# Optimization experiments

Measured on AMD Instinct MI355X. Metric: run time of the kernel, lower is better.

## Reference

```python
import jax, jax.numpy as jnp
import numpy as np

G = 32            # gridsize
N = G * G         # num_nodes = 1024
F_IN = 32         # input_dim
H = 256           # hidden_dim
L = 4             # n_layers
B = 64            # batch
MID = F_IN + L * H
MIN_VAL = -10000000.0
EPS_LN = 1e-5
EPS_BN = 1e-5


def _grid_edges():
    ids = np.arange(N).reshape(G, G)
    hs, hd = ids[:, :-1].ravel(), ids[:, 1:].ravel()
    vs, vd = ids[:-1, :].ravel(), ids[1:, :].ravel()
    src = np.concatenate([hs, hd, vs, vd]).astype(np.int32)
    dst = np.concatenate([hd, hs, vd, vs]).astype(np.int32)
    return jnp.asarray(src), jnp.asarray(dst)


def setup_inputs() -> dict:
    key = jax.random.key(0)
    ks = jax.random.split(key, 16)
    mask_f = jax.random.bernoulli(ks[0], 0.7, (B, N)).astype(jnp.float32)
    feats = jax.random.normal(ks[1], (B, N * F_IN), dtype=jnp.float32)
    observations = jnp.concatenate([mask_f, feats], axis=1)
    src, dst = _grid_edges()
    def lin(k, fi, fo):
        return jax.random.normal(k, (fi, fo), dtype=jnp.float32) / np.sqrt(fi)
    W0 = lin(ks[2], F_IN, H); b0 = jnp.zeros((H,), jnp.float32)
    g0 = jnp.ones((H,), jnp.float32); be0 = jnp.zeros((H,), jnp.float32)
    Ws = jax.random.normal(ks[3], (L - 1, H, H), jnp.float32) / np.sqrt(H)
    bs = jnp.zeros((L - 1, H), jnp.float32)
    gs = jnp.ones((L - 1, H), jnp.float32); bes = jnp.zeros((L - 1, H), jnp.float32)
    W1 = lin(ks[4], MID, 2 * H); b1 = jnp.zeros((2 * H,), jnp.float32)
    bn_g = jnp.ones((2 * H,), jnp.float32); bn_b = jnp.zeros((2 * H,), jnp.float32)
    bn_m = jax.random.normal(ks[5], (2 * H,), jnp.float32) * 0.1
    bn_v = jax.random.uniform(ks[6], (2 * H,), jnp.float32, 0.5, 1.5)
    W2 = lin(ks[7], 2 * H, 1); b2 = jnp.zeros((1,), jnp.float32)
    return {"observations": observations, "src": src, "dst": dst,
            "W0": W0, "b0": b0, "g0": g0, "be0": be0,
            "Ws": Ws, "bs": bs, "gs": gs, "bes": bes,
            "W1": W1, "b1": b1, "bn_g": bn_g, "bn_b": bn_b,
            "bn_m": bn_m, "bn_v": bn_v, "W2": W2, "b2": b2}


def _layer_norm(z, g, b):
    mu = z.mean(-1, keepdims=True)
    var = z.var(-1, keepdims=True)
    return (z - mu) / jnp.sqrt(var + EPS_LN) * g + b


def reference(observations, src, dst, W0, b0, g0, be0, Ws, bs, gs, bes,
              W1, b1, bn_g, bn_b, bn_m, bn_v, W2, b2):
    mask = observations[:, :N] != 0.0                      # [B,N] bool action mask
    x = observations[:, N:].reshape(B, N, F_IN)            # node features
    outs = [x]
    h = x
    for l in range(L):
        # GIN with eps=-1: (1+eps)*x_i vanishes -> mlp(sum of neighbor features)
        agg = jnp.zeros_like(h).at[:, dst, :].add(h[:, src, :])
        W, bb, g, be = ((W0, b0, g0, be0) if l == 0
                        else (Ws[l - 1], bs[l - 1], gs[l - 1], bes[l - 1]))
        h = jax.nn.relu(_layer_norm(agg @ W + bb, g, be))  # mlp ReLU; outer .relu() is idempotent
        outs.append(h)
    xc = jnp.concatenate(outs, axis=-1).reshape(B * N, MID)
    z = xc @ W1 + b1
    z = (z - bn_m) / jnp.sqrt(bn_v + EPS_BN) * bn_g + bn_b  # BatchNorm1d eval mode
    z = jax.nn.relu(z)                                       # dropout off in eval
    y = (z @ W2 + b2).reshape(B, N)
    return jnp.where(mask, y, MIN_VAL)
```

## Files before the change

### kernel.cpp

```cpp
#include <hip/hip_runtime.h>
#include <stdint.h>

#define FIN 32
#define HD 256
#define MIDK 1056
#define HF 512
#define MROWS 65536
#define OBS_STRIDE 33792

typedef float f32x2 __attribute__((ext_vector_type(2)));
typedef float f32x4 __attribute__((ext_vector_type(4)));

__device__ __forceinline__ unsigned pack4fp8(float a, float b, float c, float d) {
    int w = __builtin_amdgcn_cvt_pk_fp8_f32(a, b, 0, false);
    return (unsigned)__builtin_amdgcn_cvt_pk_fp8_f32(c, d, w, true);
}
__device__ __forceinline__ unsigned char f2fp8(float f) {
    return (unsigned char)(__builtin_amdgcn_cvt_pk_fp8_f32(f, f, 0, false) & 0xff);
}

__device__ __forceinline__ void glds16(const void* g, void* l) {
    __builtin_amdgcn_global_load_lds(
        (const __attribute__((address_space(1))) unsigned int*)g,
        (__attribute__((address_space(3))) unsigned int*)l,
        16, 0, 0);
}

__device__ __forceinline__ void gather16(const float* __restrict__ src, int stride, int n,
                                         unsigned char* __restrict__ dst) {
    float f[16];
#pragma unroll
    for (int j = 0; j < 16; ++j) f[j] = src[(size_t)j * stride + n];
    uint4 o;
    o.x = pack4fp8(f[0],  f[1],  f[2],  f[3]);
    o.y = pack4fp8(f[4],  f[5],  f[6],  f[7]);
    o.z = pack4fp8(f[8],  f[9],  f[10], f[11]);
    o.w = pack4fp8(f[12], f[13], f[14], f[15]);
    *(uint4*)dst = o;
}

__global__ __launch_bounds__(256) void k_prep_w(
        const float* __restrict__ W0, const float* __restrict__ Ws,
        const float* __restrict__ W1,
        unsigned char* __restrict__ Wt0, unsigned char* __restrict__ WtL,
        unsigned char* __restrict__ WtF) {
    const int b = blockIdx.x, t = threadIdx.x;
    if (b < 2) {
        int s = b * 256 + t;
        int hh = s >> 8, n = s & 255;
        gather16(W0 + (size_t)(hh * 16) * HD, HD, n, Wt0 + (size_t)s * 16);
    } else if (b < 50) {
        int u = (b - 2) * 256 + t;
        int l = u >> 12, s = u & 4095;
        int kb = s >> 9, hh = (s >> 8) & 1, n = s & 255;
        gather16(Ws + (size_t)l * 65536 + (size_t)(kb * 32 + hh * 16) * HD, HD, n,
                 WtL + (size_t)l * 65536 + (size_t)s * 16);
    } else {
        int s = (b - 50) * 256 + t;
        int kb = s >> 11, hh = (s >> 9) & 3, n = s & 511;
        int k0 = kb * 64 + hh * 16;
        if (k0 < MIDK)
            gather16(W1 + (size_t)k0 * HF, HF, n, WtF + (size_t)s * 16);
        else
            *(uint4*)(WtF + (size_t)s * 16) = make_uint4(0, 0, 0, 0);
    }
}

template <int K>
__global__ __launch_bounds__(256, 4) void k_layer(
        const unsigned char* __restrict__ Hin,
        const float* __restrict__ obs,
        const unsigned char* __restrict__ Wt,
        const float* __restrict__ bias, const float* __restrict__ gamma,
        const float* __restrict__ beta, unsigned char* __restrict__ Hout) {
    constexpr int KB = K / 32;
    __shared__ __align__(16) unsigned char Agg[(K / 16) * 64 * 16];
    __shared__ float ls[64], lss[64];
    const int t = threadIdx.x;
    const int w = t >> 6, lane = t & 63, quad = lane >> 4, l15 = lane & 15;
    const int q1 = quad >> 1, q0 = quad & 1;
    const int m0 = ((blockIdx.x & 7) * 128 + (blockIdx.x >> 3)) * 64;
    if (t < 64) { ls[t] = 0.f; lss[t] = 0.f; }

    if constexpr (K == 256) {
        const int r32 = t >> 3, seg = t & 7;
        const size_t rowBase = (size_t)(m0 & ~1023);
#pragma unroll
        for (int p = 0; p < 2; ++p) {
            const int r = p * 32 + r32;
            const int node = (m0 + r) & 1023;
            const int rr = node >> 5, cc = node & 31;
            float s[32];
#pragma unroll
            for (int i = 0; i < 32; ++i) s[i] = 0.f;
            auto addn = [&](int nn) {
                const uint4* pp = (const uint4*)(Hin + (rowBase + nn) * (size_t)K + seg * 32);
                uint4 u0 = pp[0], u1 = pp[1];
                unsigned uu[8] = {u0.x, u0.y, u0.z, u0.w, u1.x, u1.y, u1.z, u1.w};
#pragma unroll
                for (int i = 0; i < 8; ++i) {
                    f32x2 lo = __builtin_amdgcn_cvt_pk_f32_fp8(uu[i], false);
                    f32x2 hi = __builtin_amdgcn_cvt_pk_f32_fp8(uu[i], true);
                    s[4 * i + 0] += lo.x; s[4 * i + 1] += lo.y;
                    s[4 * i + 2] += hi.x; s[4 * i + 3] += hi.y;
                }
            };
            if (cc > 0)  addn(node - 1);
            if (cc < 31) addn(node + 1);
            if (rr > 0)  addn(node - 32);
            if (rr < 31) addn(node + 32);
            unsigned ow[8];
#pragma unroll
            for (int i = 0; i < 8; ++i)
                ow[i] = pack4fp8(s[4 * i], s[4 * i + 1], s[4 * i + 2], s[4 * i + 3]);
            ((uint4*)Agg)[(2 * seg) * 64 + r]     = make_uint4(ow[0], ow[1], ow[2], ow[3]);
            ((uint4*)Agg)[(2 * seg + 1) * 64 + r] = make_uint4(ow[4], ow[5], ow[6], ow[7]);
        }
    } else {
        const int r = t >> 2, seg4 = t & 3;
        const int bimg = m0 >> 10;
        const int node = (m0 + r) & 1023;
        const int rr = node >> 5, cc = node & 31;
        const float* fb = obs + (size_t)bimg * OBS_STRIDE + 1024 + seg4 * 8;
        float s[8] = {0, 0, 0, 0, 0, 0, 0, 0};
        auto addnf = [&](int nn) {
            const float4* fp = (const float4*)(fb + nn * 32);
            float4 f0 = fp[0], f1 = fp[1];
            s[0] += f0.x; s[1] += f0.y; s[2] += f0.z; s[3] += f0.w;
            s[4] += f1.x; s[5] += f1.y; s[6] += f1.z; s[7] += f1.w;
        };
        if (cc > 0)  addnf(node - 1);
        if (cc < 31) addnf(node + 1);
        if (rr > 0)  addnf(node - 32);
        if (rr < 31) addnf(node + 32);
        uint2 o;
        o.x = pack4fp8(s[0], s[1], s[2], s[3]);
        o.y = pack4fp8(s[4], s[5], s[6], s[7]);
        *(uint2*)(Agg + ((seg4 >> 1) * 64 + r) * 16 + (seg4 & 1) * 8) = o;
    }
    __syncthreads();

    f32x4 acc[4][4] = {};
#pragma unroll
    for (int kb = 0; kb < KB; ++kb) {
        long long af[4], bf[4];
        const unsigned char* bp = Wt + ((size_t)(kb * 512 + q1 * 256 + w * 64 + l15)) * 16 + q0 * 8;
#pragma unroll
        for (int nt = 0; nt < 4; ++nt)
            bf[nt] = *(const long long*)(bp + nt * 256);
#pragma unroll
        for (int mt = 0; mt < 4; ++mt)
            af[mt] = *(const long long*)(Agg + ((2 * kb + q1) * 64 + mt * 16 + l15) * 16 + q0 * 8);
#pragma unroll
        for (int mt = 0; mt < 4; ++mt)
#pragma unroll
            for (int nt = 0; nt < 4; ++nt)
                acc[mt][nt] = __builtin_amdgcn_mfma_f32_16x16x32_fp8_fp8(af[mt], bf[nt], acc[mt][nt], 0, 0, 0);
    }

#pragma unroll
    for (int mt = 0; mt < 4; ++mt) {
        float s0 = 0, s1 = 0, s2 = 0, s3 = 0, u0 = 0, u1 = 0, u2 = 0, u3 = 0;
#pragma unroll
        for (int nt = 0; nt < 4; ++nt) {
            int col = w * 64 + nt * 16 + l15;
            float bv = bias[col];
            f32x4 vv = acc[mt][nt];
            vv.x += bv; vv.y += bv; vv.z += bv; vv.w += bv;
            acc[mt][nt] = vv;
            s0 += vv.x; u0 += vv.x * vv.x;
            s1 += vv.y; u1 += vv.y * vv.y;
            s2 += vv.z; u2 += vv.z * vv.z;
            s3 += vv.w; u3 += vv.w * vv.w;
        }
#pragma unroll
        for (int msk = 1; msk < 16; msk <<= 1) {
            s0 += __shfl_xor(s0, msk); u0 += __shfl_xor(u0, msk);
            s1 += __shfl_xor(s1, msk); u1 += __shfl_xor(u1, msk);
            s2 += __shfl_xor(s2, msk); u2 += __shfl_xor(u2, msk);
            s3 += __shfl_xor(s3, msk); u3 += __shfl_xor(u3, msk);
        }
        if (l15 == 0) {
            int rl = mt * 16 + quad * 4;
            atomicAdd(&ls[rl + 0], s0); atomicAdd(&lss[rl + 0], u0);
            atomicAdd(&ls[rl + 1], s1); atomicAdd(&lss[rl + 1], u1);
            atomicAdd(&ls[rl + 2], s2); atomicAdd(&lss[rl + 2], u2);
            atomicAdd(&ls[rl + 3], s3); atomicAdd(&lss[rl + 3], u3);
        }
    }
    __syncthreads();
#pragma unroll
    for (int mt = 0; mt < 4; ++mt) {
        int rl = mt * 16 + quad * 4;
        float mu0 = ls[rl + 0] * (1.f / 256.f), mu1 = ls[rl + 1] * (1.f / 256.f);
        float mu2 = ls[rl + 2] * (1.f / 256.f), mu3 = ls[rl + 3] * (1.f / 256.f);
        float rs0 = rsqrtf(lss[rl + 0] * (1.f / 256.f) - mu0 * mu0 + 1e-5f);
        float rs1 = rsqrtf(lss[rl + 1] * (1.f / 256.f) - mu1 * mu1 + 1e-5f);
        float rs2 = rsqrtf(lss[rl + 2] * (1.f / 256.f) - mu2 * mu2 + 1e-5f);
        float rs3 = rsqrtf(lss[rl + 3] * (1.f / 256.f) - mu3 * mu3 + 1e-5f);
#pragma unroll
        for (int nt = 0; nt < 4; ++nt) {
            int col = w * 64 + nt * 16 + l15;
            float gg = gamma[col], be = beta[col];
            f32x4 vv = acc[mt][nt];
            size_t rb = (size_t)(m0 + mt * 16 + quad * 4) * HD + col;
            Hout[rb]          = f2fp8(fmaxf((vv.x - mu0) * rs0 * gg + be, 0.f));
            Hout[rb + HD]     = f2fp8(fmaxf((vv.y - mu1) * rs1 * gg + be, 0.f));
            Hout[rb + 2 * HD] = f2fp8(fmaxf((vv.z - mu2) * rs2 * gg + be, 0.f));
            Hout[rb + 3 * HD] = f2fp8(fmaxf((vv.w - mu3) * rs3 * gg + be, 0.f));
        }
    }
}

__global__ __launch_bounds__(512, 4) void k_final(
        const unsigned char* __restrict__ h0, const unsigned char* __restrict__ h1,
        const unsigned char* __restrict__ h2, const unsigned char* __restrict__ h3,
        const unsigned char* __restrict__ WtF,
        const float* __restrict__ b1,
        const float* __restrict__ bng, const float* __restrict__ bnb,
        const float* __restrict__ bnm, const float* __restrict__ bnv,
        const float* __restrict__ W2, const float* __restrict__ b2,
        const float* __restrict__ obs, float* __restrict__ out) {
    __shared__ __align__(16) unsigned char As[64 * 65 * 16];
    __shared__ __align__(16) unsigned char As2[64 * 2 * 16];
    __shared__ float yred[64];
    const int t = threadIdx.x;
    const int w = t >> 6, lane = t & 63, quad = lane >> 4, l15 = lane & 15;
    const int q1 = quad >> 1, q0 = quad & 1;
    const int wr = w >> 2, wc = w & 3;
    const int m0 = ((blockIdx.x & 7) * 128 + (blockIdx.x >> 3)) * 64;
    const int bimg = m0 >> 10, node0 = m0 & 1023;
    if (t < 64) yred[t] = 0.f;

    const unsigned char* hbuf[4] = {h0, h1, h2, h3};
    {
        const unsigned char* hb = hbuf[lane >> 4];
        const int colo = (lane & 15) * 16;
#pragma unroll
        for (int i = 0; i < 8; ++i) {
            int r = i * 8 + w;
            glds16(hb + (size_t)(m0 + r) * HD + colo, As + (size_t)r * 65 * 16);
        }
    }
    if (t < 128) {
        int h = t >> 6, r = t & 63;
        const float* p = obs + (size_t)bimg * OBS_STRIDE + 1024 + (node0 + r) * 32 + h * 16;
        float4 f0 = *(const float4*)p, f1 = *(const float4*)(p + 4);
        float4 f2 = *(const float4*)(p + 8), f3 = *(const float4*)(p + 12);
        uint4 o;
        o.x = pack4fp8(f0.x, f0.y, f0.z, f0.w);
        o.y = pack4fp8(f1.x, f1.y, f1.z, f1.w);
        o.z = pack4fp8(f2.x, f2.y, f2.z, f2.w);
        o.w = pack4fp8(f3.x, f3.y, f3.z, f3.w);
        *(uint4*)(As2 + (r * 2 + h) * 16) = o;
    }
    __syncthreads();

    f32x4 acc[2][8] = {};
    {
        long long af[2], bf[8];
        const unsigned char* bp = WtF + ((size_t)(q1 * 512 + wc * 128 + l15)) * 16 + q0 * 8;
#pragma unroll
        for (int nt = 0; nt < 8; ++nt)
            bf[nt] = *(const long long*)(bp + nt * 256);
#pragma unroll
        for (int mt = 0; mt < 2; ++mt) {
            int r = wr * 32 + mt * 16 + l15;
            af[mt] = *(const long long*)(As2 + (r * 2 + q1) * 16 + q0 * 8);
        }
#pragma unroll
        for (int mt = 0; mt < 2; ++mt)
#pragma unroll
            for (int nt = 0; nt < 8; ++nt)
                acc[mt][nt] = __builtin_amdgcn_mfma_f32_16x16x32_fp8_fp8(af[mt], bf[nt], acc[mt][nt], 0, 0, 0);
    }
    for (int c = 1; c < 33; ++c) {
        long long af[2], bf[8];
        const unsigned char* bp = WtF + ((size_t)(c * 1024 + q1 * 512 + wc * 128 + l15)) * 16 + q0 * 8;
#pragma unroll
        for (int nt = 0; nt < 8; ++nt)
            bf[nt] = *(const long long*)(bp + nt * 256);
#pragma unroll
        for (int mt = 0; mt < 2; ++mt) {
            int r = wr * 32 + mt * 16 + l15;
            af[mt] = *(const long long*)(As + ((size_t)r * 65 + 2 * (c - 1) + q1) * 16 + q0 * 8);
        }
#pragma unroll
        for (int mt = 0; mt < 2; ++mt)
#pragma unroll
            for (int nt = 0; nt < 8; ++nt)
                acc[mt][nt] = __builtin_amdgcn_mfma_f32_16x16x32_fp8_fp8(af[mt], bf[nt], acc[mt][nt], 0, 0, 0);
    }

    float scv[8], sbv[8], w2v[8];
#pragma unroll
    for (int nt = 0; nt < 8; ++nt) {
        int col = wc * 128 + nt * 16 + l15;
        float sc = bng[col] * rsqrtf(bnv[col] + 1e-5f);
        scv[nt] = sc;
        sbv[nt] = (b1[col] - bnm[col]) * sc + bnb[col];
        w2v[nt] = W2[col];
    }
#pragma unroll
    for (int mt = 0; mt < 2; ++mt) {
        float p0 = 0, p1 = 0, p2 = 0, p3 = 0;
#pragma unroll
        for (int nt = 0; nt < 8; ++nt) {
            f32x4 vv = acc[mt][nt];
            p0 += fmaxf(vv.x * scv[nt] + sbv[nt], 0.f) * w2v[nt];
            p1 += fmaxf(vv.y * scv[nt] + sbv[nt], 0.f) * w2v[nt];
            p2 += fmaxf(vv.z * scv[nt] + sbv[nt], 0.f) * w2v[nt];
            p3 += fmaxf(vv.w * scv[nt] + sbv[nt], 0.f) * w2v[nt];
        }
#pragma unroll
        for (int msk = 1; msk < 16; msk <<= 1) {
            p0 += __shfl_xor(p0, msk);
            p1 += __shfl_xor(p1, msk);
            p2 += __shfl_xor(p2, msk);
            p3 += __shfl_xor(p3, msk);
        }
        if (l15 == 0) {
            int rl = wr * 32 + mt * 16 + quad * 4;
            atomicAdd(&yred[rl + 0], p0);
            atomicAdd(&yred[rl + 1], p1);
            atomicAdd(&yred[rl + 2], p2);
            atomicAdd(&yred[rl + 3], p3);
        }
    }
    __syncthreads();
    if (t < 64) {
        int gm = m0 + t;
        float mk = obs[(size_t)bimg * OBS_STRIDE + (node0 + t)];
        out[gm] = (mk != 0.f) ? yred[t] + b2[0] : -10000000.0f;
    }
}

extern "C" void kernel_launch(void* const* d_in, const int* in_sizes, int n_in,
                              void* d_out, int out_size, void* d_ws, size_t ws_size,
                              hipStream_t stream) {
    const float* obs = (const float*)d_in[0];
    const float* W0  = (const float*)d_in[3];
    const float* b0  = (const float*)d_in[4];
    const float* g0  = (const float*)d_in[5];
    const float* be0 = (const float*)d_in[6];
    const float* Ws  = (const float*)d_in[7];
    const float* bs  = (const float*)d_in[8];
    const float* gs  = (const float*)d_in[9];
    const float* bes = (const float*)d_in[10];
    const float* W1  = (const float*)d_in[11];
    const float* b1  = (const float*)d_in[12];
    const float* bng = (const float*)d_in[13];
    const float* bnb = (const float*)d_in[14];
    const float* bnm = (const float*)d_in[15];
    const float* bnv = (const float*)d_in[16];
    const float* W2  = (const float*)d_in[17];
    const float* b2  = (const float*)d_in[18];
    float* out = (float*)d_out;

    char* ws = (char*)d_ws;
    unsigned char* h0  = (unsigned char*)(ws);
    unsigned char* h1  = (unsigned char*)(ws + 16777216);
    unsigned char* h2  = (unsigned char*)(ws + 33554432);
    unsigned char* h3  = (unsigned char*)(ws + 50331648);
    unsigned char* Wt0 = (unsigned char*)(ws + 67108864);
    unsigned char* WtL = (unsigned char*)(ws + 67117056);
    unsigned char* WtF = (unsigned char*)(ws + 67313664);

    k_prep_w<<<182, 256, 0, stream>>>(W0, Ws, W1, Wt0, WtL, WtF);

    k_layer<FIN><<<1024, 256, 0, stream>>>(h0 , obs, Wt0, b0, g0, be0, h0);
    k_layer<HD> <<<1024, 256, 0, stream>>>(h0, obs, WtL,              bs,       gs,       bes,       h1);
    k_layer<HD> <<<1024, 256, 0, stream>>>(h1, obs, WtL + 65536,      bs + 256, gs + 256, bes + 256, h2);
    k_layer<HD> <<<1024, 256, 0, stream>>>(h2, obs, WtL + 2 * 65536,  bs + 512, gs + 512, bes + 512, h3);

    k_final<<<1024, 512, 0, stream>>>(h0, h1, h2, h3, WtF, b1, bng, bnb, bnm, bnv,
                                      W2, b2, obs, out);
}
```

Before: 244.5 us.

## Double-buffer weight fragments in GEMMs and shrink final-kernel row tile to 32

In the layer kernel, the K loop now software-pipelines the B-fragment global loads into two register buffers so the next chunk's weights load while the current MFMAs run. The final kernel drops from 64 to 32 rows per block, doubles the grid, and has each of 8 waves cover 64 output columns over all 32 rows. It also merges the fp8 input-feature tile into the same padded LDS array, raises occupancy in launch bounds, and applies the same double-buffered weight loading. The cost is that each weight fragment is reused across fewer rows, so global weight traffic goes up in exchange for more parallelism and latency hiding.

```diff
diff --git a/kernel.cpp b/kernel.cpp
--- a/kernel.cpp
+++ b/kernel.cpp
@@ -141,22 +141,39 @@
     __syncthreads();
 
     f32x4 acc[4][4] = {};
-#pragma unroll
-    for (int kb = 0; kb < KB; ++kb) {
-        long long af[4], bf[4];
-        const unsigned char* bp = Wt + ((size_t)(kb * 512 + q1 * 256 + w * 64 + l15)) * 16 + q0 * 8;
-#pragma unroll
-        for (int nt = 0; nt < 4; ++nt)
-            bf[nt] = *(const long long*)(bp + nt * 256);
-#pragma unroll
-        for (int mt = 0; mt < 4; ++mt)
-            af[mt] = *(const long long*)(Agg + ((2 * kb + q1) * 64 + mt * 16 + l15) * 16 + q0 * 8);
-#pragma unroll
-        for (int mt = 0; mt < 4; ++mt)
-#pragma unroll
-            for (int nt = 0; nt < 4; ++nt)
-                acc[mt][nt] = __builtin_amdgcn_mfma_f32_16x16x32_fp8_fp8(af[mt], bf[nt], acc[mt][nt], 0, 0, 0);
-    }
+    const unsigned char* bbase = Wt + ((size_t)(q1 * 256 + w * 64 + l15)) * 16 + q0 * 8;
+    const unsigned char* abase = Agg + ((size_t)(q1 * 64 + l15)) * 16 + q0 * 8;
+
+#define LOADBL(dst, kb) { const unsigned char* bp = bbase + (size_t)(kb) * 8192; \
+    dst[0] = *(const long long*)(bp);        dst[1] = *(const long long*)(bp + 256); \
+    dst[2] = *(const long long*)(bp + 512);  dst[3] = *(const long long*)(bp + 768); }
+#define MFMAL(buf, kb) { long long af[4]; \
+    _Pragma("unroll") for (int mt = 0; mt < 4; ++mt) \
+        af[mt] = *(const long long*)(abase + (kb) * 2048 + mt * 256); \
+    _Pragma("unroll") for (int mt = 0; mt < 4; ++mt) \
+    _Pragma("unroll") for (int nt = 0; nt < 4; ++nt) \
+        acc[mt][nt] = __builtin_amdgcn_mfma_f32_16x16x32_fp8_fp8(af[mt], buf[nt], acc[mt][nt], 0, 0, 0); }
+
+    if constexpr (KB == 1) {
+        long long bA[4];
+        LOADBL(bA, 0);
+        MFMAL(bA, 0);
+    } else {
+        long long bA[4], bB[4];
+        LOADBL(bA, 0);
+#pragma unroll
+        for (int j = 0; j < KB / 2 - 1; ++j) {
+            LOADBL(bB, 2 * j + 1);
+            MFMAL(bA, 2 * j);
+            LOADBL(bA, 2 * j + 2);
+            MFMAL(bB, 2 * j + 1);
+        }
+        LOADBL(bB, KB - 1);
+        MFMAL(bA, KB - 2);
+        MFMAL(bB, KB - 1);
+    }
+#undef LOADBL
+#undef MFMAL
 
 #pragma unroll
     for (int mt = 0; mt < 4; ++mt) {
@@ -212,7 +229,7 @@
     }
 }
 
-__global__ __launch_bounds__(512, 4) void k_final(
+__global__ __launch_bounds__(512, 6) void k_final(
         const unsigned char* __restrict__ h0, const unsigned char* __restrict__ h1,
         const unsigned char* __restrict__ h2, const unsigned char* __restrict__ h3,
         const unsigned char* __restrict__ WtF,
@@ -221,30 +238,28 @@
         const float* __restrict__ bnm, const float* __restrict__ bnv,
         const float* __restrict__ W2, const float* __restrict__ b2,
         const float* __restrict__ obs, float* __restrict__ out) {
-    __shared__ __align__(16) unsigned char As[64 * 65 * 16];
-    __shared__ __align__(16) unsigned char As2[64 * 2 * 16];
-    __shared__ float yred[64];
+    __shared__ __align__(16) unsigned char As[32 * 67 * 16];
+    __shared__ float yred[32];
     const int t = threadIdx.x;
     const int w = t >> 6, lane = t & 63, quad = lane >> 4, l15 = lane & 15;
     const int q1 = quad >> 1, q0 = quad & 1;
-    const int wr = w >> 2, wc = w & 3;
-    const int m0 = ((blockIdx.x & 7) * 128 + (blockIdx.x >> 3)) * 64;
+    const int m0 = ((blockIdx.x & 7) * 256 + (blockIdx.x >> 3)) * 32;
     const int bimg = m0 >> 10, node0 = m0 & 1023;
-    if (t < 64) yred[t] = 0.f;
+    if (t < 32) yred[t] = 0.f;
 
     const unsigned char* hbuf[4] = {h0, h1, h2, h3};
     {
         const unsigned char* hb = hbuf[lane >> 4];
         const int colo = (lane & 15) * 16;
 #pragma unroll
-        for (int i = 0; i < 8; ++i) {
+        for (int i = 0; i < 4; ++i) {
             int r = i * 8 + w;
-            glds16(hb + (size_t)(m0 + r) * HD + colo, As + (size_t)r * 65 * 16);
-        }
-    }
-    if (t < 128) {
-        int h = t >> 6, r = t & 63;
-        const float* p = obs + (size_t)bimg * OBS_STRIDE + 1024 + (node0 + r) * 32 + h * 16;
+            glds16(hb + (size_t)(m0 + r) * HD + colo, As + (size_t)(r * 67 + 2) * 16);
+        }
+    }
+    if (t < 64) {
+        int hh = t & 1, r = t >> 1;
+        const float* p = obs + (size_t)bimg * OBS_STRIDE + 1024 + (node0 + r) * 32 + hh * 16;
         float4 f0 = *(const float4*)p, f1 = *(const float4*)(p + 4);
         float4 f2 = *(const float4*)(p + 8), f3 = *(const float4*)(p + 12);
         uint4 o;
@@ -252,50 +267,42 @@
         o.y = pack4fp8(f1.x, f1.y, f1.z, f1.w);
         o.z = pack4fp8(f2.x, f2.y, f2.z, f2.w);
         o.w = pack4fp8(f3.x, f3.y, f3.z, f3.w);
-        *(uint4*)(As2 + (r * 2 + h) * 16) = o;
+        *(uint4*)(As + (r * 67 + hh) * 16) = o;
     }
     __syncthreads();
 
-    f32x4 acc[2][8] = {};
-    {
-        long long af[2], bf[8];
-        const unsigned char* bp = WtF + ((size_t)(q1 * 512 + wc * 128 + l15)) * 16 + q0 * 8;
-#pragma unroll
-        for (int nt = 0; nt < 8; ++nt)
-            bf[nt] = *(const long long*)(bp + nt * 256);
-#pragma unroll
-        for (int mt = 0; mt < 2; ++mt) {
-            int r = wr * 32 + mt * 16 + l15;
-            af[mt] = *(const long long*)(As2 + (r * 2 + q1) * 16 + q0 * 8);
-        }
-#pragma unroll
-        for (int mt = 0; mt < 2; ++mt)
-#pragma unroll
-            for (int nt = 0; nt < 8; ++nt)
-                acc[mt][nt] = __builtin_amdgcn_mfma_f32_16x16x32_fp8_fp8(af[mt], bf[nt], acc[mt][nt], 0, 0, 0);
-    }
-    for (int c = 1; c < 33; ++c) {
-        long long af[2], bf[8];
-        const unsigned char* bp = WtF + ((size_t)(c * 1024 + q1 * 512 + wc * 128 + l15)) * 16 + q0 * 8;
-#pragma unroll
-        for (int nt = 0; nt < 8; ++nt)
-            bf[nt] = *(const long long*)(bp + nt * 256);
-#pragma unroll
-        for (int mt = 0; mt < 2; ++mt) {
-            int r = wr * 32 + mt * 16 + l15;
-            af[mt] = *(const long long*)(As + ((size_t)r * 65 + 2 * (c - 1) + q1) * 16 + q0 * 8);
-        }
-#pragma unroll
-        for (int mt = 0; mt < 2; ++mt)
-#pragma unroll
-            for (int nt = 0; nt < 8; ++nt)
-                acc[mt][nt] = __builtin_amdgcn_mfma_f32_16x16x32_fp8_fp8(af[mt], bf[nt], acc[mt][nt], 0, 0, 0);
-    }
-
-    float scv[8], sbv[8], w2v[8];
-#pragma unroll
-    for (int nt = 0; nt < 8; ++nt) {
-        int col = wc * 128 + nt * 16 + l15;
+    f32x4 acc[2][4] = {};
+    const unsigned char* bbase = WtF + ((size_t)(q1 * 512 + w * 64 + l15)) * 16 + q0 * 8;
+    const unsigned char* abase0 = As + ((size_t)((0 * 16 + l15) * 67 + q1)) * 16 + q0 * 8;
+    const unsigned char* abase1 = As + ((size_t)((1 * 16 + l15) * 67 + q1)) * 16 + q0 * 8;
+
+#define LOADBF(dst, c) { const unsigned char* bp = bbase + (size_t)(c) * 16384; \
+    dst[0] = *(const long long*)(bp);        dst[1] = *(const long long*)(bp + 256); \
+    dst[2] = *(const long long*)(bp + 512);  dst[3] = *(const long long*)(bp + 768); }
+#define MFMAF(buf, c) { \
+    long long a0 = *(const long long*)(abase0 + (c) * 32); \
+    long long a1 = *(const long long*)(abase1 + (c) * 32); \
+    _Pragma("unroll") for (int nt = 0; nt < 4; ++nt) { \
+        acc[0][nt] = __builtin_amdgcn_mfma_f32_16x16x32_fp8_fp8(a0, buf[nt], acc[0][nt], 0, 0, 0); \
+        acc[1][nt] = __builtin_amdgcn_mfma_f32_16x16x32_fp8_fp8(a1, buf[nt], acc[1][nt], 0, 0, 0); } }
+
+    long long bA[4], bB[4];
+    LOADBF(bA, 0);
+#pragma unroll
+    for (int cc = 0; cc < 16; ++cc) {
+        LOADBF(bB, 2 * cc + 1);
+        MFMAF(bA, 2 * cc);
+        LOADBF(bA, 2 * cc + 2);
+        MFMAF(bB, 2 * cc + 1);
+    }
+    MFMAF(bA, 32);
+#undef LOADBF
+#undef MFMAF
+
+    float scv[4], sbv[4], w2v[4];
+#pragma unroll
+    for (int nt = 0; nt < 4; ++nt) {
+        int col = w * 64 + nt * 16 + l15;
         float sc = bng[col] * rsqrtf(bnv[col] + 1e-5f);
         scv[nt] = sc;
         sbv[nt] = (b1[col] - bnm[col]) * sc + bnb[col];
@@ -305,7 +312,7 @@
     for (int mt = 0; mt < 2; ++mt) {
         float p0 = 0, p1 = 0, p2 = 0, p3 = 0;
 #pragma unroll
-        for (int nt = 0; nt < 8; ++nt) {
+        for (int nt = 0; nt < 4; ++nt) {
             f32x4 vv = acc[mt][nt];
             p0 += fmaxf(vv.x * scv[nt] + sbv[nt], 0.f) * w2v[nt];
             p1 += fmaxf(vv.y * scv[nt] + sbv[nt], 0.f) * w2v[nt];
@@ -320,7 +327,7 @@
             p3 += __shfl_xor(p3, msk);
         }
         if (l15 == 0) {
-            int rl = wr * 32 + mt * 16 + quad * 4;
+            int rl = mt * 16 + quad * 4;
             atomicAdd(&yred[rl + 0], p0);
             atomicAdd(&yred[rl + 1], p1);
             atomicAdd(&yred[rl + 2], p2);
@@ -328,7 +335,7 @@
         }
     }
     __syncthreads();
-    if (t < 64) {
+    if (t < 32) {
         int gm = m0 + t;
         float mk = obs[(size_t)bimg * OBS_STRIDE + (node0 + t)];
         out[gm] = (mk != 0.f) ? yred[t] + b2[0] : -10000000.0f;
@@ -373,6 +380,6 @@
     k_layer<HD> <<<1024, 256, 0, stream>>>(h1, obs, WtL + 65536,      bs + 256, gs + 256, bes + 256, h2);
     k_layer<HD> <<<1024, 256, 0, stream>>>(h2, obs, WtL + 2 * 65536,  bs + 512, gs + 512, bes + 512, h3);
 
-    k_final<<<1024, 512, 0, stream>>>(h0, h1, h2, h3, WtF, b1, bng, bnb, bnm, bnv,
+    k_final<<<2048, 512, 0, stream>>>(h0, h1, h2, h3, WtF, b1, bng, bnb, bnm, bnv,
                                       W2, b2, obs, out);
 }
```

After: 243.8 us. No clear change (-0.3%).
